# Optimization experiments

Measured on AMD Instinct MI355X. Metric: run time of the kernel, lower is better.

Reference implementation:

```python
import jax, jax.numpy as jnp
import numpy as np

B, T, C = 1, 2048, 1024
H, KVH = 16, 4
D = C // H            # 64
KV = KVH * D          # 256
EPS = 1e-6
SCALE = 1.0 / np.sqrt(D)
ROPE_BASE = 10000.0


def setup_inputs() -> dict:
    key = jax.random.key(0)
    ks = jax.random.split(key, 8)
    s = 0.02
    return dict(
        x=jax.random.normal(ks[0], (B, T, C), jnp.float32),
        Wq=jax.random.normal(ks[1], (C, C), jnp.float32) * s,
        Wk=jax.random.normal(ks[2], (KV, C), jnp.float32) * s,
        Wv=jax.random.normal(ks[3], (KV, C), jnp.float32) * s,
        Wo=jax.random.normal(ks[4], (C, C), jnp.float32) * s,
        q_norm_w=jnp.ones((C,), jnp.float32),
        k_norm_w=jnp.ones((KV,), jnp.float32),
        fgate_w=jax.random.normal(ks[5], (H, C), jnp.float32) * s,
        fgate_b=jnp.zeros((H,), jnp.float32),
        weight_lambda=jax.random.normal(ks[6], (C, H), jnp.float32) * s,
    )


def _rmsnorm(x, w):
    var = jnp.mean(x * x, axis=-1, keepdims=True)
    return x * jax.lax.rsqrt(var + EPS) * w


def _rotate_half(x):
    x1, x2 = jnp.split(x, 2, axis=-1)
    return jnp.concatenate([-x2, x1], axis=-1)


def _apply_rope(q, k):
    # q: [B,H,T,D], k: [B,KVH,T,D]; position_ids = arange(T)
    inv_freq = 1.0 / (ROPE_BASE ** (jnp.arange(0, D, 2, dtype=jnp.float32) / D))
    freqs = jnp.outer(jnp.arange(T, dtype=jnp.float32), inv_freq)  # [T, D/2]
    emb = jnp.concatenate([freqs, freqs], axis=-1)                 # [T, D]
    cos = jnp.cos(emb)[None, None]                                  # [1,1,T,D]
    sin = jnp.sin(emb)[None, None]
    return q * cos + _rotate_half(q) * sin, k * cos + _rotate_half(k) * sin


def _forward(x, Wq, Wk, Wv, Wo, q_norm_w, k_norm_w, fgate_w, fgate_b, weight_lambda):
    q = _rmsnorm(x @ Wq.T, q_norm_w)          # [B,T,C]
    k = _rmsnorm(x @ Wk.T, k_norm_w)          # [B,T,KV]
    v = x @ Wv.T                              # [B,T,KV]
    q = q.reshape(B, T, H, D).transpose(0, 2, 1, 3)     # [B,H,T,D]
    k = k.reshape(B, T, KVH, D).transpose(0, 2, 1, 3)   # [B,KVH,T,D]
    v = v.reshape(B, T, KVH, D).transpose(0, 2, 1, 3)
    q, k = _apply_rope(q, k)
    # GQA: repeat_interleave kv heads
    g = H // KVH
    k = jnp.repeat(k, g, axis=1)              # [B,H,T,D]
    v = jnp.repeat(v, g, axis=1)
    # Forgetting gate (FoX): log f_t per head, with elu-based lambda scaling
    lam = jax.nn.elu(x @ weight_lambda) + 1.0            # [B,T,H]
    logit = (x @ fgate_w.T + fgate_b) * lam              # [B,T,H]
    log_f = (jax.nn.log_sigmoid(logit) / (lam + 1e-3)).transpose(0, 2, 1)  # [B,H,T]
    c = jnp.cumsum(log_f, axis=-1)                       # [B,H,T]
    bias = c[..., :, None] - c[..., None, :]             # [B,H,T,T]: sum_{t=j+1..i} log f_t
    scores = jnp.einsum('bhid,bhjd->bhij', q, k) * SCALE + bias
    causal = jnp.tril(jnp.ones((T, T), dtype=bool))
    scores = jnp.where(causal, scores, -jnp.inf)
    p = jax.nn.softmax(scores, axis=-1)
    y = jnp.einsum('bhij,bhjd->bhid', p, v)              # [B,H,T,D]
    y = y.transpose(0, 2, 1, 3).reshape(B, T, C)
    return y @ Wo.T


def reference(x, Wq, Wk, Wv, Wo, q_norm_w, k_norm_w, fgate_w, fgate_b, weight_lambda):
    return _forward(x, Wq, Wk, Wv, Wo, q_norm_w, k_norm_w, fgate_w, fgate_b, weight_lambda)
```

## Files before the change

### kernel.cpp

```cpp
#include <hip/hip_runtime.h>

typedef __bf16 bf16x8 __attribute__((ext_vector_type(8)));
typedef float f32x4 __attribute__((ext_vector_type(4)));

#define MFMA_BF16 __builtin_amdgcn_mfma_f32_16x16x32_bf16

static constexpr int T_ = 2048;
static constexpr int C_ = 1024;
static constexpr int H_ = 16;
static constexpr int KVH_ = 4;
static constexpr int D_ = 64;
static constexpr float SCALE_ = 0.125f;
static constexpr float MSHIFT_ = 10.0f;

__device__ inline void cvt8(__bf16* dst, const float* src) {
  float4 a = *(const float4*)src;
  float4 b = *(const float4*)(src + 4);
  bf16x8 r;
  r[0] = (__bf16)a.x; r[1] = (__bf16)a.y; r[2] = (__bf16)a.z; r[3] = (__bf16)a.w;
  r[4] = (__bf16)b.x; r[5] = (__bf16)b.y; r[6] = (__bf16)b.z; r[7] = (__bf16)b.w;
  *(bf16x8*)dst = r;
}

__global__ __launch_bounds__(256) void cvt_kernel(
    const float* __restrict__ x,  const float* __restrict__ wq,
    const float* __restrict__ wk, const float* __restrict__ wv,
    const float* __restrict__ wo, const float* __restrict__ wl,
    __bf16* __restrict__ xb,  __bf16* __restrict__ wqb,
    __bf16* __restrict__ wkb, __bf16* __restrict__ wvb,
    __bf16* __restrict__ wob, float* __restrict__ wlT)
{
  size_t i8 = ((size_t)blockIdx.x * 256 + threadIdx.x) * 8;
  if (i8 < 2097152)       cvt8(xb  + i8,            x  + i8);
  else if (i8 < 3145728)  cvt8(wqb + (i8-2097152),  wq + (i8-2097152));
  else if (i8 < 3407872)  cvt8(wkb + (i8-3145728),  wk + (i8-3145728));
  else if (i8 < 3670016)  cvt8(wvb + (i8-3407872),  wv + (i8-3407872));
  else if (i8 < 4718592)  cvt8(wob + (i8-3670016),  wo + (i8-3670016));
  else {
    size_t r = i8 - 4718592;
    if (r < 16384) {
#pragma unroll
      for (int j = 0; j < 8; ++j) {
        size_t idx = r + j;
        size_t hh = idx >> 10, c = idx & 1023;
        wlT[idx] = wl[c * 16 + hh];
      }
    }
  }
}

template <int BM>
__global__ __launch_bounds__(256) void gemm_bt_kernel(
    const __bf16* __restrict__ A, int K, int N,
    const __bf16* __restrict__ B0, int e0,
    const __bf16* __restrict__ B1, int e1,
    const __bf16* __restrict__ B2,
    float* __restrict__ outF)
{
  __shared__ __bf16 la[BM * 40];
  __shared__ __bf16 lb[128 * 40];
  const int m0 = blockIdx.y * BM;
  const int n0 = blockIdx.x * 128;
  const __bf16* Bs; int nrel;
  if (n0 < e0)      { Bs = B0; nrel = n0; }
  else if (n0 < e1) { Bs = B1; nrel = n0 - e0; }
  else              { Bs = B2; nrel = n0 - e1; }
  const int tid = threadIdx.x;
  const int arow = tid >> 2, acol = (tid & 3) * 8;
  const __bf16* ap = A  + (size_t)(m0   + arow) * K + acol;
  const __bf16* bp = Bs + (size_t)(nrel + arow) * K + acol;
  const int w = tid >> 6, lane = tid & 63, lq = lane >> 4, ln = lane & 15;
  const int wm = (w >> 1) * (BM / 2), wn = (w & 1) * 64;
  constexpr int FM = BM / 32;
  f32x4 acc[FM][4] = {};
  for (int k0 = 0; k0 < K; k0 += 32) {
    bf16x8 a0 = *(const bf16x8*)(ap + k0);
    bf16x8 a1{};
    if (BM == 128) a1 = *(const bf16x8*)(ap + (size_t)64 * K + k0);
    bf16x8 b0 = *(const bf16x8*)(bp + k0);
    bf16x8 b1 = *(const bf16x8*)(bp + (size_t)64 * K + k0);
    __syncthreads();
    *(bf16x8*)(la + arow * 40 + acol) = a0;
    if (BM == 128) *(bf16x8*)(la + (arow + 64) * 40 + acol) = a1;
    *(bf16x8*)(lb + arow * 40 + acol) = b0;
    *(bf16x8*)(lb + (arow + 64) * 40 + acol) = b1;
    __syncthreads();
    bf16x8 af[FM], bfr[4];
#pragma unroll
    for (int i = 0; i < FM; ++i)
      af[i] = *(const bf16x8*)(la + (wm + i * 16 + ln) * 40 + lq * 8);
#pragma unroll
    for (int j = 0; j < 4; ++j)
      bfr[j] = *(const bf16x8*)(lb + (wn + j * 16 + ln) * 40 + lq * 8);
#pragma unroll
    for (int i = 0; i < FM; ++i)
#pragma unroll
      for (int j = 0; j < 4; ++j)
        acc[i][j] = MFMA_BF16(af[i], bfr[j], acc[i][j], 0, 0, 0);
  }
#pragma unroll
  for (int i = 0; i < FM; ++i)
#pragma unroll
    for (int j = 0; j < 4; ++j)
#pragma unroll
      for (int r = 0; r < 4; ++r) {
        int row = m0 + wm + i * 16 + lq * 4 + r;
        int col = n0 + wn + j * 16 + ln;
        outF[(size_t)row * N + col] = acc[i][j][r];
      }
}

__global__ __launch_bounds__(256) void gates_kernel(
    const float* __restrict__ x, const float* __restrict__ fw,
    const float* __restrict__ fb, const float* __restrict__ wlT,
    float* __restrict__ logf)
{
  const int t = blockIdx.x;
  const int tid = threadIdx.x, w = tid >> 6, lane = tid & 63;
  float xv[16];
#pragma unroll
  for (int i = 0; i < 16; ++i)
    xv[i] = x[(size_t)t * C_ + i * 64 + lane];
#pragma unroll
  for (int u = 0; u < 4; ++u) {
    int h = w * 4 + u;
    float s1 = 0.f, s2 = 0.f;
#pragma unroll
    for (int i = 0; i < 16; ++i) {
      int cidx = i * 64 + lane;
      s1 += xv[i] * wlT[(size_t)h * C_ + cidx];
      s2 += xv[i] * fw[(size_t)h * C_ + cidx];
    }
    for (int m = 32; m; m >>= 1) {
      s1 += __shfl_xor(s1, m);
      s2 += __shfl_xor(s2, m);
    }
    if (lane == 0) {
      float lam = (s1 > 0.f ? s1 : expm1f(s1)) + 1.0f;
      float logit = (s2 + fb[h]) * lam;
      float ls = (logit >= 0.f) ? -log1pf(expf(-logit))
                                : (logit - log1pf(expf(logit)));
      logf[(size_t)h * T_ + t] = ls / (lam + 1e-3f);
    }
  }
}

__global__ __launch_bounds__(64) void cumsum_kernel(
    const float* __restrict__ logf, float* __restrict__ csum)
{
  const int h = blockIdx.x;
  const int lane = threadIdx.x;
  float carry = 0.f;
  for (int ch = 0; ch < T_ / 64; ++ch) {
    float v = logf[(size_t)h * T_ + ch * 64 + lane];
#pragma unroll
    for (int d = 1; d < 64; d <<= 1) {
      float tv = __shfl_up(v, d);
      if (lane >= d) v += tv;
    }
    v += carry;
    csum[(size_t)h * T_ + ch * 64 + lane] = v;
    carry = __shfl(v, 63);
  }
}

__global__ __launch_bounds__(256) void normrope_kernel(
    const float* __restrict__ qkv, const float* __restrict__ qw,
    const float* __restrict__ kw, __bf16* __restrict__ qh,
    __bf16* __restrict__ kh, __bf16* __restrict__ vh)
{
  const int t = blockIdx.x, tid = threadIdx.x;
  __shared__ float qn[1024];
  __shared__ float kn[256];
  __shared__ float red[16];
  __shared__ float rc[32], rs[32];
  if (tid < 32) {
    float fr = (float)t * exp2f((float)tid * -0.41524101186404527f);
    float sn, cs;
    sincosf(fr, &sn, &cs);
    rc[tid] = cs; rs[tid] = sn;
  }
  const float* row = qkv + (size_t)t * 1536;
  float4 q4 = *(const float4*)(row + tid * 4);
  float kvl = row[1024 + tid];
  float vvl = row[1280 + tid];
  float ssq = q4.x * q4.x + q4.y * q4.y + q4.z * q4.z + q4.w * q4.w;
  float ssk = kvl * kvl;
  const int lane = tid & 63, w = tid >> 6;
  for (int m = 32; m; m >>= 1) {
    ssq += __shfl_xor(ssq, m);
    ssk += __shfl_xor(ssk, m);
  }
  if (lane == 0) { red[w] = ssq; red[8 + w] = ssk; }
  __syncthreads();
  float sq = red[0] + red[1] + red[2] + red[3];
  float sk = red[8] + red[9] + red[10] + red[11];
  float rq = rsqrtf(sq * (1.0f / 1024.f) + 1e-6f);
  float rk = rsqrtf(sk * (1.0f / 256.f) + 1e-6f);
  qn[tid * 4 + 0] = q4.x * rq * qw[tid * 4 + 0];
  qn[tid * 4 + 1] = q4.y * rq * qw[tid * 4 + 1];
  qn[tid * 4 + 2] = q4.z * rq * qw[tid * 4 + 2];
  qn[tid * 4 + 3] = q4.w * rq * qw[tid * 4 + 3];
  kn[tid] = kvl * rk * kw[tid];
  __syncthreads();
#pragma unroll
  for (int u = 0; u < 4; ++u) {
    int cidx = tid * 4 + u;
    int hh = cidx >> 6, d = cidx & 63, i = d & 31;
    float cs = rc[i], sn = rs[i];
    float val = (d < 32) ? (qn[cidx] * cs - qn[cidx + 32] * sn)
                         : (qn[cidx] * cs + qn[cidx - 32] * sn);
    qh[(size_t)hh * T_ * D_ + (size_t)t * D_ + d] = (__bf16)val;
  }
  {
    int d = tid & 63, kvhh = tid >> 6, i = d & 31;
    float cs = rc[i], sn = rs[i];
    float kval = (d < 32) ? (kn[tid] * cs - kn[tid + 32] * sn)
                          : (kn[tid] * cs + kn[tid - 32] * sn);
    kh[(size_t)kvhh * T_ * D_ + (size_t)t * D_ + d] = (__bf16)kval;
    vh[(size_t)kvhh * T_ * D_ + (size_t)t * D_ + d] = (__bf16)vvl;
  }
}

__global__ __launch_bounds__(256) void vtrans_kernel(
    const __bf16* __restrict__ vh, __bf16* __restrict__ vt)
{
  const int tb = blockIdx.x, kvh = blockIdx.y;
  __shared__ __bf16 tile[64][72];
  const int tid = threadIdx.x;
  const int r = tid >> 2, cb = (tid & 3) * 16;
  const __bf16* src = vh + (size_t)kvh * T_ * D_ + (size_t)(tb * 64 + r) * D_ + cb;
  bf16x8 v0 = *(const bf16x8*)(src);
  bf16x8 v1 = *(const bf16x8*)(src + 8);
  *(bf16x8*)(&tile[r][cb]) = v0;
  *(bf16x8*)(&tile[r][cb + 8]) = v1;
  __syncthreads();
  bf16x8 o0, o1;
#pragma unroll
  for (int j = 0; j < 8; ++j) o0[j] = tile[cb + j][r];
#pragma unroll
  for (int j = 0; j < 8; ++j) o1[j] = tile[cb + 8 + j][r];
  __bf16* dst = vt + (size_t)kvh * D_ * T_ + (size_t)r * T_ + tb * 64 + cb;
  *(bf16x8*)(dst) = o0;
  *(bf16x8*)(dst + 8) = o1;
}

__global__ __launch_bounds__(256) void attn_kernel(
    const __bf16* __restrict__ qh, const __bf16* __restrict__ kh,
    const __bf16* __restrict__ vt, const float* __restrict__ csum,
    __bf16* __restrict__ y)
{
  const int ib = blockIdx.x, h = blockIdx.y;
  const int i0 = ib * 64, kvh = h >> 2;
  __shared__ __bf16 kt[64 * 72];
  __shared__ __bf16 vtt[64 * 72];
  __shared__ __bf16 pt[4][16 * 72];
  const int tid = threadIdx.x;
  const int w = tid >> 6, lane = tid & 63, lq = lane >> 4, ln = lane & 15;
  const int srow = tid >> 2, scol = (tid & 3) * 16;
  const __bf16* kbase = kh + (size_t)kvh * T_ * D_;
  const __bf16* vbase = vt + (size_t)kvh * D_ * T_;
  const __bf16* qp = qh + ((size_t)h * T_ + i0 + w * 16 + ln) * D_;
  bf16x8 aq0 = *(const bf16x8*)(qp + lq * 8);
  bf16x8 aq1 = *(const bf16x8*)(qp + 32 + lq * 8);
  float ci[4];
#pragma unroll
  for (int r = 0; r < 4; ++r)
    ci[r] = csum[(size_t)h * T_ + i0 + w * 16 + lq * 4 + r];
  f32x4 o[4] = {};
  f32x4 ls = {0.f, 0.f, 0.f, 0.f};
  bf16x8 ones;
#pragma unroll
  for (int j = 0; j < 8; ++j) ones[j] = (__bf16)1.0f;
  __bf16* pw = &pt[w][0];

  bf16x8 kr0 = *(const bf16x8*)(kbase + (size_t)srow * D_ + scol);
  bf16x8 kr1 = *(const bf16x8*)(kbase + (size_t)srow * D_ + scol + 8);
  bf16x8 vr0 = *(const bf16x8*)(vbase + (size_t)srow * T_ + scol);
  bf16x8 vr1 = *(const bf16x8*)(vbase + (size_t)srow * T_ + scol + 8);
  *(bf16x8*)(kt + srow * 72 + scol) = kr0;
  *(bf16x8*)(kt + srow * 72 + scol + 8) = kr1;
  *(bf16x8*)(vtt + srow * 72 + scol) = vr0;
  *(bf16x8*)(vtt + srow * 72 + scol + 8) = vr1;
  __syncthreads();

  auto tilebody = [&](int j0, bool diag) {
    f32x4 s[4];
    const f32x4 zf = {0.f, 0.f, 0.f, 0.f};
#pragma unroll
    for (int jj = 0; jj < 4; ++jj) {
      bf16x8 bk0 = *(const bf16x8*)(kt + (jj * 16 + ln) * 72 + lq * 8);
      bf16x8 bk1 = *(const bf16x8*)(kt + (jj * 16 + ln) * 72 + 32 + lq * 8);
      s[jj] = MFMA_BF16(aq0, bk0, zf, 0, 0, 0);
      s[jj] = MFMA_BF16(aq1, bk1, s[jj], 0, 0, 0);
    }
    float cj[4];
#pragma unroll
    for (int jj = 0; jj < 4; ++jj)
      cj[jj] = csum[(size_t)h * T_ + j0 + jj * 16 + ln];
#pragma unroll
    for (int jj = 0; jj < 4; ++jj)
#pragma unroll
      for (int r = 0; r < 4; ++r) {
        float arg = fmaf(s[jj][r], SCALE_, ci[r] - cj[jj] - MSHIFT_);
        float p = __expf(arg);
        if (diag && (jj * 16 + ln > w * 16 + lq * 4 + r)) p = 0.f;
        pw[(lq * 4 + r) * 72 + jj * 16 + ln] = (__bf16)p;
      }
    asm volatile("s_waitcnt lgkmcnt(0)" ::: "memory");
    bf16x8 pa0 = *(const bf16x8*)(pw + ln * 72 + lq * 8);
    bf16x8 pa1 = *(const bf16x8*)(pw + ln * 72 + 32 + lq * 8);
    ls = MFMA_BF16(pa0, ones, ls, 0, 0, 0);
    ls = MFMA_BF16(pa1, ones, ls, 0, 0, 0);
#pragma unroll
    for (int dd = 0; dd < 4; ++dd) {
      bf16x8 bv0 = *(const bf16x8*)(vtt + (dd * 16 + ln) * 72 + lq * 8);
      bf16x8 bv1 = *(const bf16x8*)(vtt + (dd * 16 + ln) * 72 + 32 + lq * 8);
      o[dd] = MFMA_BF16(pa0, bv0, o[dd], 0, 0, 0);
      o[dd] = MFMA_BF16(pa1, bv1, o[dd], 0, 0, 0);
    }
  };

  for (int jt = 0; jt < ib; ++jt) {
    const int j0n = (jt + 1) * 64;
    kr0 = *(const bf16x8*)(kbase + (size_t)(j0n + srow) * D_ + scol);
    kr1 = *(const bf16x8*)(kbase + (size_t)(j0n + srow) * D_ + scol + 8);
    vr0 = *(const bf16x8*)(vbase + (size_t)srow * T_ + j0n + scol);
    vr1 = *(const bf16x8*)(vbase + (size_t)srow * T_ + j0n + scol + 8);
    tilebody(jt * 64, false);
    __syncthreads();
    *(bf16x8*)(kt + srow * 72 + scol) = kr0;
    *(bf16x8*)(kt + srow * 72 + scol + 8) = kr1;
    *(bf16x8*)(vtt + srow * 72 + scol) = vr0;
    *(bf16x8*)(vtt + srow * 72 + scol + 8) = vr1;
    __syncthreads();
  }
  tilebody(i0, true);

#pragma unroll
  for (int dd = 0; dd < 4; ++dd)
#pragma unroll
    for (int r = 0; r < 4; ++r) {
      int iabs = i0 + w * 16 + lq * 4 + r;
      int col = h * 64 + dd * 16 + ln;
      y[(size_t)iabs * C_ + col] = (__bf16)(o[dd][r] / ls[r]);
    }
}

extern "C" void kernel_launch(void* const* d_in, const int* in_sizes, int n_in,
                              void* d_out, int out_size, void* d_ws, size_t ws_size,
                              hipStream_t stream) {
  const float* x   = (const float*)d_in[0];
  const float* Wq  = (const float*)d_in[1];
  const float* Wk  = (const float*)d_in[2];
  const float* Wv  = (const float*)d_in[3];
  const float* Wo  = (const float*)d_in[4];
  const float* qnw = (const float*)d_in[5];
  const float* knw = (const float*)d_in[6];
  const float* fgw = (const float*)d_in[7];
  const float* fgb = (const float*)d_in[8];
  const float* wl  = (const float*)d_in[9];

  char* ws = (char*)d_ws;
  size_t off = 0;
  float*  qkv  = (float*)(ws + off);  off += (size_t)T_ * 1536 * 4;
  float*  logf = (float*)(ws + off);  off += (size_t)H_ * T_ * 4;
  float*  csum = (float*)(ws + off);  off += (size_t)H_ * T_ * 4;
  __bf16* qh   = (__bf16*)(ws + off); off += (size_t)H_ * T_ * D_ * 2;
  __bf16* kh   = (__bf16*)(ws + off); off += (size_t)KVH_ * T_ * D_ * 2;
  __bf16* vh   = (__bf16*)(ws + off); off += (size_t)KVH_ * T_ * D_ * 2;
  __bf16* vt   = (__bf16*)(ws + off); off += (size_t)KVH_ * T_ * D_ * 2;
  __bf16* y    = (__bf16*)(ws + off); off += (size_t)T_ * C_ * 2;
  __bf16* xb   = (__bf16*)(ws + off); off += (size_t)T_ * C_ * 2;
  __bf16* wqb  = (__bf16*)(ws + off); off += (size_t)C_ * C_ * 2;
  __bf16* wkb  = (__bf16*)(ws + off); off += (size_t)256 * C_ * 2;
  __bf16* wvb  = (__bf16*)(ws + off); off += (size_t)256 * C_ * 2;
  __bf16* wob  = (__bf16*)(ws + off); off += (size_t)C_ * C_ * 2;
  float*  wlT  = (float*)(ws + off);  off += (size_t)H_ * C_ * 4;

  cvt_kernel<<<2312, 256, 0, stream>>>(x, Wq, Wk, Wv, Wo, wl,
                                       xb, wqb, wkb, wvb, wob, wlT);
  gemm_bt_kernel<64><<<dim3(12, 32), 256, 0, stream>>>(
      xb, 1024, 1536, wqb, 1024, wkb, 1280, wvb, qkv);
  gates_kernel<<<T_, 256, 0, stream>>>(x, fgw, fgb, wlT, logf);
  cumsum_kernel<<<H_, 64, 0, stream>>>(logf, csum);
  normrope_kernel<<<T_, 256, 0, stream>>>(qkv, qnw, knw, qh, kh, vh);
  vtrans_kernel<<<dim3(T_ / 64, KVH_), 256, 0, stream>>>(vh, vt);
  attn_kernel<<<dim3(T_ / 64, H_), 256, 0, stream>>>(qh, kh, vt, csum, y);
  gemm_bt_kernel<64><<<dim3(8, 32), 256, 0, stream>>>(
      y, 1024, 1024, wob, 1024, wob, 1024, wob, (float*)d_out);
}
```

Before: 203.0 us.

## Split causal attention KV range into segments with atomic partial accumulation

Attention blocks now split the key range into up to four segments of eight tiles each along a new grid dimension, so long query rows are processed by several blocks in parallel. Rows that need more than one segment accumulate unnormalized outputs and row sums into fp32 buffers with atomics, and a new finalize kernel divides and writes bf16. The fp32 buffers are zeroed in the conversion kernel. This targets the load imbalance of the causal triangle and the low block count, at the cost of atomic traffic, a larger workspace and an extra launch.

```diff
diff --git a/kernel.cpp b/kernel.cpp
--- a/kernel.cpp
+++ b/kernel.cpp
@@ -28,7 +28,8 @@
     const float* __restrict__ wo, const float* __restrict__ wl,
     __bf16* __restrict__ xb,  __bf16* __restrict__ wqb,
     __bf16* __restrict__ wkb, __bf16* __restrict__ wvb,
-    __bf16* __restrict__ wob, float* __restrict__ wlT)
+    __bf16* __restrict__ wob, float* __restrict__ wlT,
+    float* __restrict__ zbuf)
 {
   size_t i8 = ((size_t)blockIdx.x * 256 + threadIdx.x) * 8;
   if (i8 < 2097152)       cvt8(xb  + i8,            x  + i8);
@@ -36,15 +37,20 @@
   else if (i8 < 3407872)  cvt8(wkb + (i8-3145728),  wk + (i8-3145728));
   else if (i8 < 3670016)  cvt8(wvb + (i8-3407872),  wv + (i8-3407872));
   else if (i8 < 4718592)  cvt8(wob + (i8-3670016),  wo + (i8-3670016));
-  else {
+  else if (i8 < 4734976) {
     size_t r = i8 - 4718592;
-    if (r < 16384) {
-#pragma unroll
-      for (int j = 0; j < 8; ++j) {
-        size_t idx = r + j;
-        size_t hh = idx >> 10, c = idx & 1023;
-        wlT[idx] = wl[c * 16 + hh];
-      }
+#pragma unroll
+    for (int j = 0; j < 8; ++j) {
+      size_t idx = r + j;
+      size_t hh = idx >> 10, c = idx & 1023;
+      wlT[idx] = wl[c * 16 + hh];
+    }
+  } else {
+    size_t z = i8 - 4734976;
+    if (z < 2129920) {
+      float4 zz = {0.f, 0.f, 0.f, 0.f};
+      *(float4*)(zbuf + z) = zz;
+      *(float4*)(zbuf + z + 4) = zz;
     }
   }
 }
@@ -248,10 +254,16 @@
 __global__ __launch_bounds__(256) void attn_kernel(
     const __bf16* __restrict__ qh, const __bf16* __restrict__ kh,
     const __bf16* __restrict__ vt, const float* __restrict__ csum,
-    __bf16* __restrict__ y)
-{
-  const int ib = blockIdx.x, h = blockIdx.y;
+    __bf16* __restrict__ y, float* __restrict__ oacc,
+    float* __restrict__ lsacc)
+{
+  const int ib = blockIdx.x, h = blockIdx.y, sg = blockIdx.z;
+  const int jt0 = sg * 8;
+  if (jt0 > ib) return;
   const int i0 = ib * 64, kvh = h >> 2;
+  const int jtend = min(jt0 + 8, ib);
+  const bool hasdiag = ((ib >> 3) == sg);
+  const int nseg = (ib >> 3) + 1;
   __shared__ __bf16 kt[64 * 72];
   __shared__ __bf16 vtt[64 * 72];
   __shared__ __bf16 pt[4][16 * 72];
@@ -274,10 +286,10 @@
   for (int j = 0; j < 8; ++j) ones[j] = (__bf16)1.0f;
   __bf16* pw = &pt[w][0];
 
-  bf16x8 kr0 = *(const bf16x8*)(kbase + (size_t)srow * D_ + scol);
-  bf16x8 kr1 = *(const bf16x8*)(kbase + (size_t)srow * D_ + scol + 8);
-  bf16x8 vr0 = *(const bf16x8*)(vbase + (size_t)srow * T_ + scol);
-  bf16x8 vr1 = *(const bf16x8*)(vbase + (size_t)srow * T_ + scol + 8);
+  bf16x8 kr0 = *(const bf16x8*)(kbase + (size_t)(jt0 * 64 + srow) * D_ + scol);
+  bf16x8 kr1 = *(const bf16x8*)(kbase + (size_t)(jt0 * 64 + srow) * D_ + scol + 8);
+  bf16x8 vr0 = *(const bf16x8*)(vbase + (size_t)srow * T_ + jt0 * 64 + scol);
+  bf16x8 vr1 = *(const bf16x8*)(vbase + (size_t)srow * T_ + jt0 * 64 + scol + 8);
   *(bf16x8*)(kt + srow * 72 + scol) = kr0;
   *(bf16x8*)(kt + srow * 72 + scol + 8) = kr1;
   *(bf16x8*)(vtt + srow * 72 + scol) = vr0;
@@ -321,30 +333,66 @@
     }
   };
 
-  for (int jt = 0; jt < ib; ++jt) {
+  for (int jt = jt0; jt < jtend; ++jt) {
+    const bool pf = (jt + 1 < jtend) || hasdiag;
     const int j0n = (jt + 1) * 64;
-    kr0 = *(const bf16x8*)(kbase + (size_t)(j0n + srow) * D_ + scol);
-    kr1 = *(const bf16x8*)(kbase + (size_t)(j0n + srow) * D_ + scol + 8);
-    vr0 = *(const bf16x8*)(vbase + (size_t)srow * T_ + j0n + scol);
-    vr1 = *(const bf16x8*)(vbase + (size_t)srow * T_ + j0n + scol + 8);
+    if (pf) {
+      kr0 = *(const bf16x8*)(kbase + (size_t)(j0n + srow) * D_ + scol);
+      kr1 = *(const bf16x8*)(kbase + (size_t)(j0n + srow) * D_ + scol + 8);
+      vr0 = *(const bf16x8*)(vbase + (size_t)srow * T_ + j0n + scol);
+      vr1 = *(const bf16x8*)(vbase + (size_t)srow * T_ + j0n + scol + 8);
+    }
     tilebody(jt * 64, false);
-    __syncthreads();
-    *(bf16x8*)(kt + srow * 72 + scol) = kr0;
-    *(bf16x8*)(kt + srow * 72 + scol + 8) = kr1;
-    *(bf16x8*)(vtt + srow * 72 + scol) = vr0;
-    *(bf16x8*)(vtt + srow * 72 + scol + 8) = vr1;
-    __syncthreads();
-  }
-  tilebody(i0, true);
-
-#pragma unroll
-  for (int dd = 0; dd < 4; ++dd)
-#pragma unroll
-    for (int r = 0; r < 4; ++r) {
-      int iabs = i0 + w * 16 + lq * 4 + r;
-      int col = h * 64 + dd * 16 + ln;
-      y[(size_t)iabs * C_ + col] = (__bf16)(o[dd][r] / ls[r]);
-    }
+    if (pf) {
+      __syncthreads();
+      *(bf16x8*)(kt + srow * 72 + scol) = kr0;
+      *(bf16x8*)(kt + srow * 72 + scol + 8) = kr1;
+      *(bf16x8*)(vtt + srow * 72 + scol) = vr0;
+      *(bf16x8*)(vtt + srow * 72 + scol + 8) = vr1;
+      __syncthreads();
+    }
+  }
+  if (hasdiag) tilebody(i0, true);
+
+  if (nseg == 1) {
+#pragma unroll
+    for (int dd = 0; dd < 4; ++dd)
+#pragma unroll
+      for (int r = 0; r < 4; ++r) {
+        int iabs = i0 + w * 16 + lq * 4 + r;
+        int col = h * 64 + dd * 16 + ln;
+        y[(size_t)iabs * C_ + col] = (__bf16)(o[dd][r] / ls[r]);
+      }
+  } else {
+#pragma unroll
+    for (int dd = 0; dd < 4; ++dd)
+#pragma unroll
+      for (int r = 0; r < 4; ++r) {
+        int iabs = i0 + w * 16 + lq * 4 + r;
+        atomicAdd(oacc + ((size_t)h * T_ + iabs) * D_ + dd * 16 + ln, o[dd][r]);
+      }
+    if (ln == 0) {
+#pragma unroll
+      for (int r = 0; r < 4; ++r)
+        atomicAdd(lsacc + (size_t)h * T_ + i0 + w * 16 + lq * 4 + r, ls[r]);
+    }
+  }
+}
+
+__global__ __launch_bounds__(256) void attnfin_kernel(
+    const float* __restrict__ oacc, const float* __restrict__ lsacc,
+    __bf16* __restrict__ y)
+{
+  const int t = 512 + blockIdx.x;
+  const int c = threadIdx.x * 4;
+  const int h = c >> 6, d = c & 63;
+  float inv = 1.0f / lsacc[(size_t)h * T_ + t];
+  float4 o4 = *(const float4*)(oacc + ((size_t)h * T_ + t) * D_ + d);
+  __bf16* yp = y + (size_t)t * C_ + c;
+  yp[0] = (__bf16)(o4.x * inv);
+  yp[1] = (__bf16)(o4.y * inv);
+  yp[2] = (__bf16)(o4.z * inv);
+  yp[3] = (__bf16)(o4.w * inv);
 }
 
 extern "C" void kernel_launch(void* const* d_in, const int* in_sizes, int n_in,
@@ -377,16 +425,20 @@
   __bf16* wvb  = (__bf16*)(ws + off); off += (size_t)256 * C_ * 2;
   __bf16* wob  = (__bf16*)(ws + off); off += (size_t)C_ * C_ * 2;
   float*  wlT  = (float*)(ws + off);  off += (size_t)H_ * C_ * 4;
-
-  cvt_kernel<<<2312, 256, 0, stream>>>(x, Wq, Wk, Wv, Wo, wl,
-                                       xb, wqb, wkb, wvb, wob, wlT);
+  float*  oacc = (float*)(ws + off);  off += (size_t)H_ * T_ * D_ * 4;
+  float*  lsacc= (float*)(ws + off);  off += (size_t)H_ * T_ * 4;
+
+  cvt_kernel<<<3352, 256, 0, stream>>>(x, Wq, Wk, Wv, Wo, wl,
+                                       xb, wqb, wkb, wvb, wob, wlT, oacc);
   gemm_bt_kernel<64><<<dim3(12, 32), 256, 0, stream>>>(
       xb, 1024, 1536, wqb, 1024, wkb, 1280, wvb, qkv);
   gates_kernel<<<T_, 256, 0, stream>>>(x, fgw, fgb, wlT, logf);
   cumsum_kernel<<<H_, 64, 0, stream>>>(logf, csum);
   normrope_kernel<<<T_, 256, 0, stream>>>(qkv, qnw, knw, qh, kh, vh);
   vtrans_kernel<<<dim3(T_ / 64, KVH_), 256, 0, stream>>>(vh, vt);
-  attn_kernel<<<dim3(T_ / 64, H_), 256, 0, stream>>>(qh, kh, vt, csum, y);
+  attn_kernel<<<dim3(T_ / 64, H_, 4), 256, 0, stream>>>(qh, kh, vt, csum, y,
+                                                        oacc, lsacc);
+  attnfin_kernel<<<T_ - 512, 256, 0, stream>>>(oacc, lsacc, y);
   gemm_bt_kernel<64><<<dim3(8, 32), 256, 0, stream>>>(
       y, 1024, 1024, wob, 1024, wob, 1024, wob, (float*)d_out);
 }
```

Result: no change. 203.2 us (+0.1%).
